# Kernel tuning notes

Hardware: AMD Instinct MI355X
Metric: run time of the kernel (lower is better)

The kernel has to match this reference:

```python
import jax, jax.numpy as jnp
import numpy as np

B, T, H, E = 8, 2048, 512, 512

def setup_inputs() -> dict:
    key = jax.random.key(0)
    k1, k2, k3, k4 = jax.random.split(key, 4)
    tokens = jax.random.normal(k1, (B, T, H), dtype=jnp.float32)
    # Linear(hidden,embed,bias=False): stored as (in,out) so Q = tokens @ Wq
    Wq = jax.random.normal(k2, (H, E), dtype=jnp.float32) / np.sqrt(H)
    Wk = jax.random.normal(k3, (H, E), dtype=jnp.float32) / np.sqrt(H)
    Wv = jax.random.normal(k4, (H, H), dtype=jnp.float32) / np.sqrt(H)
    return {"tokens": tokens, "Wq": Wq, "Wk": Wk, "Wv": Wv}

def reference(tokens, Wq, Wk, Wv):
    Q = jnp.einsum('bth,he->bte', tokens, Wq)   # [B,T,E]
    K = jnp.einsum('bsh,he->bse', tokens, Wk)   # [B,T,E]
    V = jnp.einsum('bsh,hd->bsd', tokens, Wv)   # [B,T,H]
    scoremats = jnp.einsum('bte,bse->bts', Q, K)  # [B,T,T]
    # NOTE: softmax over axis=1 (query axis t), matching F.softmax(dim=1)
    attnmats = jax.nn.softmax(scoremats, axis=1)
    ctx_vecs = jnp.einsum('bts,bsh->bth', attnmats, V)  # [B,T,H]
    return ctx_vecs
```

## Files before the change

kernel.cpp:

```cpp
#include <hip/hip_runtime.h>

typedef _Float16 f16;
typedef _Float16 f16x8 __attribute__((ext_vector_type(8)));
typedef _Float16 f16x4 __attribute__((ext_vector_type(4)));
typedef float   f32x4 __attribute__((ext_vector_type(4)));

#define LOG2E 1.44269504088896340736f

__device__ __forceinline__ f32x4 mfma_f16(f16x8 a, f16x8 b, f32x4 c){
  return __builtin_amdgcn_mfma_f32_16x16x32_f16(a, b, c, 0, 0, 0);
}
__device__ __forceinline__ float fexp2(float x){ return __builtin_amdgcn_exp2f(x); }

__device__ __forceinline__ void gld16(void* lds, const void* g){
  __builtin_amdgcn_global_load_lds(
      (const __attribute__((address_space(1))) unsigned int*)g,
      (__attribute__((address_space(3))) unsigned int*)lds,
      16, 0, 0);
}

__global__ __launch_bounds__(256) void k_prep_g(const float* __restrict__ Wq,
                                                const float* __restrict__ Wk,
                                                f16* __restrict__ B16){
  __shared__ float ak[32][36];
  __shared__ float aq[32][36];
  const int n0 = blockIdx.y * 32, e0 = blockIdx.x * 32;
  const int u = threadIdx.x;
  const int ty = u >> 4, tx = u & 15;
  float acc[2][2] = {};
  for (int x0 = 0; x0 < 512; x0 += 32){
    __syncthreads();
    {
      int r = u >> 3, c4 = (u & 7) * 4;
      *(float4*)&ak[r][c4] = *(const float4*)&Wk[(n0 + r) * 512 + x0 + c4];
      *(float4*)&aq[r][c4] = *(const float4*)&Wq[(e0 + r) * 512 + x0 + c4];
    }
    __syncthreads();
#pragma unroll 8
    for (int x = 0; x < 32; ++x){
      float k0 = ak[ty * 2 + 0][x], k1 = ak[ty * 2 + 1][x];
      float q0 = aq[tx * 2 + 0][x], q1 = aq[tx * 2 + 1][x];
      acc[0][0] += k0 * q0; acc[0][1] += k0 * q1;
      acc[1][0] += k1 * q0; acc[1][1] += k1 * q1;
    }
  }
#pragma unroll
  for (int i = 0; i < 2; ++i)
#pragma unroll
    for (int j = 0; j < 2; ++j)
      B16[(size_t)(n0 + ty * 2 + i) * 512 + e0 + tx * 2 + j] = (f16)acc[i][j];
}

__global__ __launch_bounds__(256) void k_prep_wv(const float* __restrict__ Wv,
                                                 f16* __restrict__ B16){
  __shared__ float t[64][72];
  const int e0 = blockIdx.x * 64, h0 = blockIdx.y * 64;
  const int u = threadIdx.x;
#pragma unroll
  for (int k = 0; k < 4; ++k){
    int idx = u + k * 256; int r = idx >> 4, c4 = (idx & 15) * 4;
    *(float4*)&t[r][c4] = *(const float4*)&Wv[(e0 + r) * 512 + h0 + c4];
  }
  __syncthreads();
#pragma unroll
  for (int k = 0; k < 4; ++k){
    int idx = u + k * 256; int j = idx >> 4, i4 = (idx & 15) * 4;
#pragma unroll
    for (int c = 0; c < 4; ++c)
      B16[(size_t)(512 + h0 + j) * 512 + e0 + i4 + c] = (f16)t[i4 + c][j];
  }
}

__global__ __launch_bounds__(256) void k_cast(const float* __restrict__ tok,
                                              f16* __restrict__ T16){
  int i = blockIdx.x * 256 + threadIdx.x;
  const float4* p = (const float4*)tok + (size_t)i * 2;
  float4 a = p[0], b = p[1];
  f16x8 h;
  h[0] = (f16)a.x; h[1] = (f16)a.y; h[2] = (f16)a.z; h[3] = (f16)a.w;
  h[4] = (f16)b.x; h[5] = (f16)b.y; h[6] = (f16)b.z; h[7] = (f16)b.w;
  *((f16x8*)T16 + i) = h;
}

__global__ __launch_bounds__(256, 4) void k_gemm(const f16* __restrict__ T16,
                                                 const f16* __restrict__ B16,
                                                 f16* __restrict__ QG,
                                                 f16* __restrict__ VT){
  __shared__ __align__(16) f16 Abuf[2][128 * 32];
  __shared__ __align__(16) f16 Bbuf[2][128 * 32];
  const int tb = blockIdx.x, nb = blockIdx.y;
  const int u = threadIdx.x;
  const int w = u >> 6, l = u & 63, lr = l & 15, lq = l >> 4;
  const int l2 = l & 3, hi4 = l >> 2;
  const int wm = (w & 1) * 64, wn = (w >> 1) * 64;
  f32x4 acc[4][4] = {};
  auto stage = [&](int c, int buf){
    const f16* sa = T16 + (size_t)tb * 128 * 512 + c * 32;
    const f16* sb = B16 + (size_t)nb * 128 * 512 + c * 32;
#pragma unroll
    for (int k = 0; k < 2; ++k){
      int i = w * 2 + k;
      int row = i * 16 + hi4;
      gld16((char*)&Abuf[buf][0] + i * 1024, sa + (size_t)row * 512 + ((l2 ^ (row & 3)) * 8));
      gld16((char*)&Bbuf[buf][0] + i * 1024, sb + (size_t)row * 512 + ((l2 ^ (row & 3)) * 8));
    }
  };
  stage(0, 0);
  for (int c = 0; c < 16; ++c){
    __syncthreads();
    if (c < 15) stage(c + 1, (c + 1) & 1);
    const f16* A = &Abuf[c & 1][0];
    const f16* B = &Bbuf[c & 1][0];
    f16x8 af[4], bf[4];
#pragma unroll
    for (int mt = 0; mt < 4; ++mt){
      int row = wm + mt * 16 + lr;
      af[mt] = *(const f16x8*)((const char*)A + row * 64 + ((lq ^ (row & 3)) << 4));
    }
#pragma unroll
    for (int nt = 0; nt < 4; ++nt){
      int row = wn + nt * 16 + lr;
      bf[nt] = *(const f16x8*)((const char*)B + row * 64 + ((lq ^ (row & 3)) << 4));
    }
#pragma unroll
    for (int mt = 0; mt < 4; ++mt)
#pragma unroll
      for (int nt = 0; nt < 4; ++nt)
        acc[mt][nt] = mfma_f16(af[mt], bf[nt], acc[mt][nt]);
  }
  if (nb < 4){
#pragma unroll
    for (int mt = 0; mt < 4; ++mt)
#pragma unroll
      for (int nt = 0; nt < 4; ++nt){
        int n = nb * 128 + wn + nt * 16 + lr;
        int r0 = tb * 128 + wm + mt * 16 + lq * 4;
#pragma unroll
        for (int j = 0; j < 4; ++j)
          QG[(size_t)(r0 + j) * 512 + n] = (f16)acc[mt][nt][j];
      }
  } else {
#pragma unroll
    for (int mt = 0; mt < 4; ++mt)
#pragma unroll
      for (int nt = 0; nt < 4; ++nt){
        int h = (nb - 4) * 128 + wn + nt * 16 + lr;
        int r0 = tb * 128 + wm + mt * 16 + lq * 4;
        int bq = r0 >> 11, s = r0 & 2047;
        f16x4 hv;
#pragma unroll
        for (int j = 0; j < 4; ++j) hv[j] = (f16)acc[mt][nt][j];
        *(f16x4*)&VT[(size_t)(bq * 512 + h) * 2048 + s] = hv;
      }
  }
}

__global__ __launch_bounds__(256, 4) void k_pass1p(const f16* __restrict__ T16,
                                                   const f16* __restrict__ QG,
                                                   f16* __restrict__ Pp,
                                                   float* __restrict__ Mp,
                                                   float* __restrict__ Dp){
  const int gid = blockIdx.x;
  const int b = gid & 7;
  const int sb = (gid >> 3) & 15;
  const int tb = gid >> 7;
  const int u = threadIdx.x;
  const int w = u >> 6, l = u & 63, lr = l & 15, lq = l >> 4;
  const int l2 = l & 3, hi4 = l >> 2;
  const int wm = (w & 1) * 64, wn = (w >> 1) * 64;

  __shared__ __align__(16) f16 Abuf[2][128 * 32];
  __shared__ __align__(16) f16 Bbuf[2][128 * 32];
  __shared__ float redM[2][128];
  __shared__ float redD[2][128];

  f32x4 acc[4][4] = {};
  auto stage = [&](int c, int buf){
    const f16* sa = T16 + ((size_t)(b * 2048 + sb * 128) * 512 + c * 32);
    const f16* sb_ = QG + ((size_t)(b * 2048 + tb * 128) * 512 + c * 32);
#pragma unroll
    for (int k = 0; k < 2; ++k){
      int i = w * 2 + k;
      int row = i * 16 + hi4;
      gld16((char*)&Abuf[buf][0] + i * 1024, sa  + (size_t)row * 512 + ((l2 ^ (row & 3)) * 8));
      gld16((char*)&Bbuf[buf][0] + i * 1024, sb_ + (size_t)row * 512 + ((l2 ^ (row & 3)) * 8));
    }
  };
  stage(0, 0);
  for (int c = 0; c < 16; ++c){
    __syncthreads();
    if (c < 15) stage(c + 1, (c + 1) & 1);
    const f16* A = &Abuf[c & 1][0];
    const f16* B = &Bbuf[c & 1][0];
    f16x8 af[4], bf[4];
#pragma unroll
    for (int mt = 0; mt < 4; ++mt){
      int row = wm + mt * 16 + lr;
      af[mt] = *(const f16x8*)((const char*)A + row * 64 + ((lq ^ (row & 3)) << 4));
    }
#pragma unroll
    for (int nt = 0; nt < 4; ++nt){
      int row = wn + nt * 16 + lr;
      bf[nt] = *(const f16x8*)((const char*)B + row * 64 + ((lq ^ (row & 3)) << 4));
    }
#pragma unroll
    for (int mt = 0; mt < 4; ++mt)
#pragma unroll
      for (int nt = 0; nt < 4; ++nt)
        acc[mt][nt] = mfma_f16(af[mt], bf[nt], acc[mt][nt]);
  }
#pragma unroll
  for (int mt = 0; mt < 4; ++mt)
#pragma unroll
    for (int nt = 0; nt < 4; ++nt)
#pragma unroll
      for (int j = 0; j < 4; ++j)
        acc[mt][nt][j] *= LOG2E;
#pragma unroll
  for (int mt = 0; mt < 4; ++mt)
#pragma unroll
    for (int j = 0; j < 4; ++j){
      float m2 = fmaxf(fmaxf(acc[mt][0][j], acc[mt][1][j]),
                       fmaxf(acc[mt][2][j], acc[mt][3][j]));
#pragma unroll
      for (int off = 1; off <= 8; off <<= 1)
        m2 = fmaxf(m2, __shfl_xor(m2, off, 64));
      if (lr == 0) redM[w >> 1][wm + mt * 16 + lq * 4 + j] = m2;
    }
  __syncthreads();
  float M[4][4];
#pragma unroll
  for (int mt = 0; mt < 4; ++mt)
#pragma unroll
    for (int j = 0; j < 4; ++j){
      int idx = wm + mt * 16 + lq * 4 + j;
      M[mt][j] = fmaxf(redM[0][idx], redM[1][idx]);
    }
#pragma unroll
  for (int mt = 0; mt < 4; ++mt)
#pragma unroll
    for (int nt = 0; nt < 4; ++nt){
      int t = tb * 128 + wn + nt * 16 + lr;
      f16x4 h4;
#pragma unroll
      for (int j = 0; j < 4; ++j){
        float p = fexp2(acc[mt][nt][j] - M[mt][j]);
        acc[mt][nt][j] = p;
        h4[j] = (f16)p;
      }
      *(f16x4*)&Pp[(size_t)(b * 2048 + t) * 2048 + sb * 128 + wm + mt * 16 + lq * 4] = h4;
    }
#pragma unroll
  for (int mt = 0; mt < 4; ++mt)
#pragma unroll
    for (int j = 0; j < 4; ++j){
      float sd = acc[mt][0][j] + acc[mt][1][j] + acc[mt][2][j] + acc[mt][3][j];
#pragma unroll
      for (int off = 1; off <= 8; off <<= 1)
        sd += __shfl_xor(sd, off, 64);
      if (lr == 0) redD[w >> 1][wm + mt * 16 + lq * 4 + j] = sd;
    }
  __syncthreads();
  if (u < 128){
    int sg = b * 2048 + sb * 128 + u;
    Mp[tb * 16384 + sg] = fmaxf(redM[0][u], redM[1][u]);
    Dp[tb * 16384 + sg] = redD[0][u] + redD[1][u];
  }
}

__global__ __launch_bounds__(256) void k_scm(const float* __restrict__ Mp,
                                             const float* __restrict__ Dp,
                                             f16* __restrict__ SC16){
  int i = blockIdx.x * 256 + threadIdx.x;
  float mv[16];
  float m = -1e30f;
#pragma unroll
  for (int ti = 0; ti < 16; ++ti){
    mv[ti] = Mp[ti * 16384 + i];
    m = fmaxf(m, mv[ti]);
  }
  float d = 0.f;
#pragma unroll
  for (int ti = 0; ti < 16; ++ti)
    d += Dp[ti * 16384 + i] * fexp2(mv[ti] - m);
  float rd = 1.0f / d;
#pragma unroll
  for (int ti = 0; ti < 16; ++ti)
    SC16[ti * 16384 + i] = (f16)(fexp2(mv[ti] - m) * rd);
}

__global__ __launch_bounds__(256, 4) void k_pass2p(const f16* __restrict__ Pp,
                                                   const f16* __restrict__ VT,
                                                   const f16* __restrict__ SC16,
                                                   float* __restrict__ out){
  const int gid = blockIdx.x;
  const int b = gid & 7;
  const int tb = (gid >> 3) & 15;
  const int hb = gid >> 7;
  const int u = threadIdx.x;
  const int w = u >> 6, l = u & 63, lr = l & 15, lq = l >> 4;
  const int l2 = l & 3, hi4 = l >> 2;
  const int wm = (w & 1) * 64, wn = (w >> 1) * 64;

  __shared__ __align__(16) f16 Abuf[2][128 * 32];
  __shared__ __align__(16) f16 Bbuf[2][128 * 32];
  __shared__ __align__(16) f16 scl[2048];

  {
    f16x8 v = *(const f16x8*)&SC16[(size_t)tb * 16384 + b * 2048 + u * 8];
    *(f16x8*)&scl[u * 8] = v;
  }
  f32x4 acc[4][4] = {};
  auto stage = [&](int c, int buf){
    const f16* sa = VT + ((size_t)(b * 512 + hb * 128) * 2048 + c * 32);
    const f16* sb_ = Pp + ((size_t)(b * 2048 + tb * 128) * 2048 + c * 32);
#pragma unroll
    for (int k = 0; k < 2; ++k){
      int i = w * 2 + k;
      int row = i * 16 + hi4;
      gld16((char*)&Abuf[buf][0] + i * 1024, sa  + (size_t)row * 2048 + ((l2 ^ (row & 3)) * 8));
      gld16((char*)&Bbuf[buf][0] + i * 1024, sb_ + (size_t)row * 2048 + ((l2 ^ (row & 3)) * 8));
    }
  };
  stage(0, 0);
  for (int c = 0; c < 64; ++c){
    __syncthreads();
    if (c < 63) stage(c + 1, (c + 1) & 1);
    const f16* A = &Abuf[c & 1][0];
    const f16* B = &Bbuf[c & 1][0];
    f16x8 sclv = *(const f16x8*)&scl[c * 32 + lq * 8];
    f16x8 af[4], bf[4];
#pragma unroll
    for (int mt = 0; mt < 4; ++mt){
      int row = wm + mt * 16 + lr;
      af[mt] = *(const f16x8*)((const char*)A + row * 64 + ((lq ^ (row & 3)) << 4));
    }
#pragma unroll
    for (int nt = 0; nt < 4; ++nt){
      int row = wn + nt * 16 + lr;
      f16x8 p = *(const f16x8*)((const char*)B + row * 64 + ((lq ^ (row & 3)) << 4));
      bf[nt] = p * sclv;
    }
#pragma unroll
    for (int mt = 0; mt < 4; ++mt)
#pragma unroll
      for (int nt = 0; nt < 4; ++nt)
        acc[mt][nt] = mfma_f16(af[mt], bf[nt], acc[mt][nt]);
  }
#pragma unroll
  for (int mt = 0; mt < 4; ++mt)
#pragma unroll
    for (int nt = 0; nt < 4; ++nt){
      int t = tb * 128 + wn + nt * 16 + lr;
      int h = hb * 128 + wm + mt * 16 + lq * 4;
      float4 v;
      v.x = acc[mt][nt][0]; v.y = acc[mt][nt][1];
      v.z = acc[mt][nt][2]; v.w = acc[mt][nt][3];
      *(float4*)&out[(size_t)(b * 2048 + t) * 512 + h] = v;
    }
}

extern "C" void kernel_launch(void* const* d_in, const int* in_sizes, int n_in,
                              void* d_out, int out_size, void* d_ws, size_t ws_size,
                              hipStream_t stream){
  (void)in_sizes; (void)n_in; (void)out_size; (void)ws_size;
  const float* tokens = (const float*)d_in[0];
  const float* Wq = (const float*)d_in[1];
  const float* Wk = (const float*)d_in[2];
  const float* Wv = (const float*)d_in[3];
  char* ws = (char*)d_ws;
  f16*    T16 = (f16*)(ws);
  f16*    QG  = (f16*)(ws + (16u << 20));
  f16*    VT  = (f16*)(ws + (32u << 20));
  f16*    B16 = (f16*)(ws + (48u << 20));
  f16*    SC16= (f16*)(ws + (50u << 20));
  float*  Mp  = (float*)(ws + (51u << 20));
  float*  Dp  = (float*)(ws + (52u << 20));
  f16*    Pp  = (f16*)(ws + (54u << 20));
  float* out = (float*)d_out;

  k_prep_g <<<dim3(16, 16), dim3(256), 0, stream>>>(Wq, Wk, B16);
  k_prep_wv<<<dim3(8, 8),   dim3(256), 0, stream>>>(Wv, B16);
  k_cast   <<<dim3(4096),   dim3(256), 0, stream>>>(tokens, T16);
  k_gemm   <<<dim3(128, 8), dim3(256), 0, stream>>>(T16, B16, QG, VT);
  k_pass1p <<<dim3(2048),   dim3(256), 0, stream>>>(T16, QG, Pp, Mp, Dp);
  k_scm    <<<dim3(64),     dim3(256), 0, stream>>>(Mp, Dp, SC16);
  k_pass2p <<<dim3(512),    dim3(256), 0, stream>>>(Pp, VT, SC16, out);
}
```

Baseline: 178.7 us.

## Triple-buffer pass1 loads with manual waitcnt barriers and change LDS swizzle

Changes the LDS XOR swizzle in all three GEMM kernels to key on (row>>1)&3 instead of row&3, aiming to cut LDS bank conflicts on the 16-byte fragment reads. In k_pass1p it also moves from double to triple buffering, prefetching two stages ahead. The __syncthreads is replaced by inline s_waitcnt vmcnt(4)/s_barrier so the next stage's loads can stay in flight. Occupancy bound drops to 3 blocks per CU to fit the larger LDS footprint, which may reduce latency hiding elsewhere.

```diff
diff --git a/kernel.cpp b/kernel.cpp
--- a/kernel.cpp
+++ b/kernel.cpp
@@ -18,6 +18,7 @@
       (__attribute__((address_space(3))) unsigned int*)lds,
       16, 0, 0);
 }
+
 
 __global__ __launch_bounds__(256) void k_prep_g(const float* __restrict__ Wq,
                                                 const float* __restrict__ Wk,
@@ -91,7 +92,7 @@
   const int tb = blockIdx.x, nb = blockIdx.y;
   const int u = threadIdx.x;
   const int w = u >> 6, l = u & 63, lr = l & 15, lq = l >> 4;
-  const int l2 = l & 3, hi4 = l >> 2;
+  const int sxor = (l & 3) ^ ((l >> 3) & 3), hi4 = l >> 2;
   const int wm = (w & 1) * 64, wn = (w >> 1) * 64;
   f32x4 acc[4][4] = {};
   auto stage = [&](int c, int buf){
@@ -101,8 +102,8 @@
     for (int k = 0; k < 2; ++k){
       int i = w * 2 + k;
       int row = i * 16 + hi4;
-      gld16((char*)&Abuf[buf][0] + i * 1024, sa + (size_t)row * 512 + ((l2 ^ (row & 3)) * 8));
-      gld16((char*)&Bbuf[buf][0] + i * 1024, sb + (size_t)row * 512 + ((l2 ^ (row & 3)) * 8));
+      gld16((char*)&Abuf[buf][0] + i * 1024, sa + (size_t)row * 512 + sxor * 8);
+      gld16((char*)&Bbuf[buf][0] + i * 1024, sb + (size_t)row * 512 + sxor * 8);
     }
   };
   stage(0, 0);
@@ -115,12 +116,12 @@
 #pragma unroll
     for (int mt = 0; mt < 4; ++mt){
       int row = wm + mt * 16 + lr;
-      af[mt] = *(const f16x8*)((const char*)A + row * 64 + ((lq ^ (row & 3)) << 4));
+      af[mt] = *(const f16x8*)((const char*)A + row * 64 + (((lq ^ ((row >> 1) & 3))) << 4));
     }
 #pragma unroll
     for (int nt = 0; nt < 4; ++nt){
       int row = wn + nt * 16 + lr;
-      bf[nt] = *(const f16x8*)((const char*)B + row * 64 + ((lq ^ (row & 3)) << 4));
+      bf[nt] = *(const f16x8*)((const char*)B + row * 64 + (((lq ^ ((row >> 1) & 3))) << 4));
     }
 #pragma unroll
     for (int mt = 0; mt < 4; ++mt)
@@ -155,7 +156,7 @@
   }
 }
 
-__global__ __launch_bounds__(256, 4) void k_pass1p(const f16* __restrict__ T16,
+__global__ __launch_bounds__(256, 3) void k_pass1p(const f16* __restrict__ T16,
                                                    const f16* __restrict__ QG,
                                                    f16* __restrict__ Pp,
                                                    float* __restrict__ Mp,
@@ -166,42 +167,47 @@
   const int tb = gid >> 7;
   const int u = threadIdx.x;
   const int w = u >> 6, l = u & 63, lr = l & 15, lq = l >> 4;
-  const int l2 = l & 3, hi4 = l >> 2;
+  const int sxor = (l & 3) ^ ((l >> 3) & 3), hi4 = l >> 2;
   const int wm = (w & 1) * 64, wn = (w >> 1) * 64;
 
-  __shared__ __align__(16) f16 Abuf[2][128 * 32];
-  __shared__ __align__(16) f16 Bbuf[2][128 * 32];
+  __shared__ __align__(16) f16 Abuf[3][128 * 32];
+  __shared__ __align__(16) f16 Bbuf[3][128 * 32];
   __shared__ float redM[2][128];
   __shared__ float redD[2][128];
 
   f32x4 acc[4][4] = {};
+  const f16* sa0 = T16 + ((size_t)(b * 2048 + sb * 128) * 512);
+  const f16* sb0 = QG + ((size_t)(b * 2048 + tb * 128) * 512);
   auto stage = [&](int c, int buf){
-    const f16* sa = T16 + ((size_t)(b * 2048 + sb * 128) * 512 + c * 32);
-    const f16* sb_ = QG + ((size_t)(b * 2048 + tb * 128) * 512 + c * 32);
+    const f16* sa = sa0 + c * 32;
+    const f16* sb_ = sb0 + c * 32;
 #pragma unroll
     for (int k = 0; k < 2; ++k){
       int i = w * 2 + k;
       int row = i * 16 + hi4;
-      gld16((char*)&Abuf[buf][0] + i * 1024, sa  + (size_t)row * 512 + ((l2 ^ (row & 3)) * 8));
-      gld16((char*)&Bbuf[buf][0] + i * 1024, sb_ + (size_t)row * 512 + ((l2 ^ (row & 3)) * 8));
+      gld16((char*)&Abuf[buf][0] + i * 1024, sa  + (size_t)row * 512 + sxor * 8);
+      gld16((char*)&Bbuf[buf][0] + i * 1024, sb_ + (size_t)row * 512 + sxor * 8);
     }
   };
   stage(0, 0);
+  stage(1, 1);
+#pragma unroll
   for (int c = 0; c < 16; ++c){
-    __syncthreads();
-    if (c < 15) stage(c + 1, (c + 1) & 1);
-    const f16* A = &Abuf[c & 1][0];
-    const f16* B = &Bbuf[c & 1][0];
+    if (c < 15) asm volatile("s_waitcnt vmcnt(4) lgkmcnt(0)\n\ts_barrier" ::: "memory");
+    else        asm volatile("s_waitcnt vmcnt(0) lgkmcnt(0)\n\ts_barrier" ::: "memory");
+    if (c + 2 < 16) stage(c + 2, (c + 2) % 3);
+    const f16* A = &Abuf[c % 3][0];
+    const f16* B = &Bbuf[c % 3][0];
     f16x8 af[4], bf[4];
 #pragma unroll
     for (int mt = 0; mt < 4; ++mt){
       int row = wm + mt * 16 + lr;
-      af[mt] = *(const f16x8*)((const char*)A + row * 64 + ((lq ^ (row & 3)) << 4));
+      af[mt] = *(const f16x8*)((const char*)A + row * 64 + (((lq ^ ((row >> 1) & 3))) << 4));
     }
 #pragma unroll
     for (int nt = 0; nt < 4; ++nt){
       int row = wn + nt * 16 + lr;
-      bf[nt] = *(const f16x8*)((const char*)B + row * 64 + ((lq ^ (row & 3)) << 4));
+      bf[nt] = *(const f16x8*)((const char*)B + row * 64 + (((lq ^ ((row >> 1) & 3))) << 4));
     }
 #pragma unroll
     for (int mt = 0; mt < 4; ++mt)
@@ -299,7 +305,7 @@
   const int hb = gid >> 7;
   const int u = threadIdx.x;
   const int w = u >> 6, l = u & 63, lr = l & 15, lq = l >> 4;
-  const int l2 = l & 3, hi4 = l >> 2;
+  const int sxor = (l & 3) ^ ((l >> 3) & 3), hi4 = l >> 2;
   const int wm = (w & 1) * 64, wn = (w >> 1) * 64;
 
   __shared__ __align__(16) f16 Abuf[2][128 * 32];
@@ -318,8 +324,8 @@
     for (int k = 0; k < 2; ++k){
       int i = w * 2 + k;
       int row = i * 16 + hi4;
-      gld16((char*)&Abuf[buf][0] + i * 1024, sa  + (size_t)row * 2048 + ((l2 ^ (row & 3)) * 8));
-      gld16((char*)&Bbuf[buf][0] + i * 1024, sb_ + (size_t)row * 2048 + ((l2 ^ (row & 3)) * 8));
+      gld16((char*)&Abuf[buf][0] + i * 1024, sa  + (size_t)row * 2048 + sxor * 8);
+      gld16((char*)&Bbuf[buf][0] + i * 1024, sb_ + (size_t)row * 2048 + sxor * 8);
     }
   };
   stage(0, 0);
@@ -333,12 +339,12 @@
 #pragma unroll
     for (int mt = 0; mt < 4; ++mt){
       int row = wm + mt * 16 + lr;
-      af[mt] = *(const f16x8*)((const char*)A + row * 64 + ((lq ^ (row & 3)) << 4));
+      af[mt] = *(const f16x8*)((const char*)A + row * 64 + (((lq ^ ((row >> 1) & 3))) << 4));
     }
 #pragma unroll
     for (int nt = 0; nt < 4; ++nt){
       int row = wn + nt * 16 + lr;
-      f16x8 p = *(const f16x8*)((const char*)B + row * 64 + ((lq ^ (row & 3)) << 4));
+      f16x8 p = *(const f16x8*)((const char*)B + row * 64 + (((lq ^ ((row >> 1) & 3))) << 4));
       bf[nt] = p * sclv;
     }
 #pragma unroll
```

Measured after the change: 176.7 us. About the same (-1.1%).
